# Kernel tuning notes

Measured on AMD Instinct MI355X. Metric: run time of the kernel, lower is better.

Reference implementation:

```python
import jax, jax.numpy as jnp
import numpy as np
import math

B, N, M, D, HID, OUT = 8, 2048, 2048, 1024, 1024, 1024

def setup_inputs() -> dict:
    key = jax.random.key(0)
    k1, k2, k3, k4, k5, k6 = jax.random.split(key, 6)
    h1 = jax.random.normal(k1, (B, N, D), dtype=jnp.float32)
    h2 = jax.random.normal(k2, (B, M, D), dtype=jnp.float32)
    mask = jax.random.randint(k3, (B, N, M), 0, 2, dtype=jnp.int32)
    # nn.Linear(in, out, bias=False) weight has shape (out, in)
    Wq = jax.random.normal(k4, (HID, D), dtype=jnp.float32) / math.sqrt(D)
    Wk = jax.random.normal(k5, (HID, D), dtype=jnp.float32) / math.sqrt(D)
    Wv = jax.random.normal(k6, (OUT, D), dtype=jnp.float32) / math.sqrt(D)
    return {"h1": h1, "h2": h2, "mask": mask, "Wq": Wq, "Wk": Wk, "Wv": Wv}

def reference(h1, h2, mask, Wq, Wk, Wv):
    Q = jnp.einsum('bnd,hd->bnh', h1, Wq)            # (B,N,HID)
    K = jnp.einsum('bmd,hd->bmh', h2, Wk)            # (B,M,HID)
    V = jnp.einsum('bmd,od->bmo', h2, Wv)            # (B,M,OUT)
    E = jnp.einsum('bnh,bmh->bnm', Q, K)             # (B,N,M) scores
    # NOTE: original masks E BEFORE dividing by sqrt(hidden_d)
    E = jnp.where(mask == 0, jnp.float32(-1e10), E)
    A = jax.nn.softmax(E / math.sqrt(HID), axis=2)
    return jnp.einsum('bnm,bmo->bno', A, V)          # (B,N,OUT)
```

## Files before the change

kernel.cpp:

```cpp
#include <hip/hip_runtime.h>


using f16   = _Float16;
using f16x4 = __attribute__((ext_vector_type(4))) _Float16;
using f16x8 = __attribute__((ext_vector_type(8))) _Float16;
using f32x4 = __attribute__((ext_vector_type(4))) float;

typedef unsigned int u32_g __attribute__((address_space(1)));
typedef unsigned int u32_l __attribute__((address_space(3)));

__device__ __forceinline__ void gl_lds16(const f16* g, f16* l) {
    __builtin_amdgcn_global_load_lds((const u32_g*)g, (u32_l*)l, 16, 0, 0);
}

#define FENCE() asm volatile("" ::: "memory")
#define BAR()   do { FENCE(); __builtin_amdgcn_s_barrier(); FENCE(); } while (0)

#define MFMA_HALF(A0_, A1_, A2_, A3_, RG_)                                               \
  do {                                                                                   \
    if constexpr (EPI == 2) {                                                            \
      rs[RG_+0] = __builtin_amdgcn_mfma_f32_16x16x32_f16(A0_, bones, rs[RG_+0], 0,0,0);  \
      rs[RG_+1] = __builtin_amdgcn_mfma_f32_16x16x32_f16(A1_, bones, rs[RG_+1], 0,0,0);  \
      rs[RG_+2] = __builtin_amdgcn_mfma_f32_16x16x32_f16(A2_, bones, rs[RG_+2], 0,0,0);  \
      rs[RG_+3] = __builtin_amdgcn_mfma_f32_16x16x32_f16(A3_, bones, rs[RG_+3], 0,0,0);  \
    }                                                                                    \
    acc[RG_+0][0] = __builtin_amdgcn_mfma_f32_16x16x32_f16(A0_, b0, acc[RG_+0][0],0,0,0);\
    acc[RG_+0][1] = __builtin_amdgcn_mfma_f32_16x16x32_f16(A0_, b1, acc[RG_+0][1],0,0,0);\
    acc[RG_+0][2] = __builtin_amdgcn_mfma_f32_16x16x32_f16(A0_, b2, acc[RG_+0][2],0,0,0);\
    acc[RG_+0][3] = __builtin_amdgcn_mfma_f32_16x16x32_f16(A0_, b3, acc[RG_+0][3],0,0,0);\
    acc[RG_+1][0] = __builtin_amdgcn_mfma_f32_16x16x32_f16(A1_, b0, acc[RG_+1][0],0,0,0);\
    acc[RG_+1][1] = __builtin_amdgcn_mfma_f32_16x16x32_f16(A1_, b1, acc[RG_+1][1],0,0,0);\
    acc[RG_+1][2] = __builtin_amdgcn_mfma_f32_16x16x32_f16(A1_, b2, acc[RG_+1][2],0,0,0);\
    acc[RG_+1][3] = __builtin_amdgcn_mfma_f32_16x16x32_f16(A1_, b3, acc[RG_+1][3],0,0,0);\
    acc[RG_+2][0] = __builtin_amdgcn_mfma_f32_16x16x32_f16(A2_, b0, acc[RG_+2][0],0,0,0);\
    acc[RG_+2][1] = __builtin_amdgcn_mfma_f32_16x16x32_f16(A2_, b1, acc[RG_+2][1],0,0,0);\
    acc[RG_+2][2] = __builtin_amdgcn_mfma_f32_16x16x32_f16(A2_, b2, acc[RG_+2][2],0,0,0);\
    acc[RG_+2][3] = __builtin_amdgcn_mfma_f32_16x16x32_f16(A2_, b3, acc[RG_+2][3],0,0,0);\
    acc[RG_+3][0] = __builtin_amdgcn_mfma_f32_16x16x32_f16(A3_, b0, acc[RG_+3][0],0,0,0);\
    acc[RG_+3][1] = __builtin_amdgcn_mfma_f32_16x16x32_f16(A3_, b1, acc[RG_+3][1],0,0,0);\
    acc[RG_+3][2] = __builtin_amdgcn_mfma_f32_16x16x32_f16(A3_, b2, acc[RG_+3][2],0,0,0);\
    acc[RG_+3][3] = __builtin_amdgcn_mfma_f32_16x16x32_f16(A3_, b3, acc[RG_+3][3],0,0,0);\
  } while (0)

#define TILE_BODY(T_, STG_, VM_)                                                         \
  {                                                                                      \
    const f16* bufA_ = smem + ((T_) & 3) * 16384;                                        \
    const f16* bufB_ = bufA_ + 8192;                                                     \
    if (STG_) {                                                                          \
      f16* dA_ = ldsAw + ((T_ + 3) & 3) * 16384;                                         \
      f16* dB_ = ldsBw + ((T_ + 3) & 3) * 16384;                                         \
      const f16* gA_ = gAs + (long)(T_ + 3) * 32;                                        \
      const f16* gB_ = gBs + (long)(T_ + 3) * 32;                                        \
      gl_lds16(gA_, dA_);                                                                \
      gl_lds16(gA_ + sweep, dA_ + 4096);                                                 \
      gl_lds16(gB_, dB_);                                                                \
      gl_lds16(gB_ + sweep, dB_ + 4096);                                                 \
    }                                                                                    \
    f16x8 a0_, a1_, a2_, a3_, a4_, a5_, a6_, a7_, b0, b1, b2, b3;                        \
    a0_ = *(const f16x8*)(bufA_ + offA);                                                 \
    a1_ = *(const f16x8*)(bufA_ + offA + 512);                                           \
    a2_ = *(const f16x8*)(bufA_ + offA + 1024);                                          \
    a3_ = *(const f16x8*)(bufA_ + offA + 1536);                                          \
    b0  = *(const f16x8*)(bufB_ + offB);                                                 \
    b1  = *(const f16x8*)(bufB_ + offB + 512);                                           \
    b2  = *(const f16x8*)(bufB_ + offB + 1024);                                          \
    b3  = *(const f16x8*)(bufB_ + offB + 1536);                                          \
    a4_ = *(const f16x8*)(bufA_ + offA + 2048);                                          \
    a5_ = *(const f16x8*)(bufA_ + offA + 2560);                                          \
    a6_ = *(const f16x8*)(bufA_ + offA + 3072);                                          \
    a7_ = *(const f16x8*)(bufA_ + offA + 3584);                                          \
    __builtin_amdgcn_s_setprio(1);                                                       \
    MFMA_HALF(a0_, a1_, a2_, a3_, 0);                                                    \
    MFMA_HALF(a4_, a5_, a6_, a7_, 4);                                                    \
    __builtin_amdgcn_s_setprio(0);                                                       \
    asm volatile(VM_ ::: "memory");                                                      \
    BAR();                                                                               \
  }

template <int EPI, int GDEC, int LGX>
__global__ __launch_bounds__(512, 2)
void gemm256_nt_f16(const f16* __restrict__ A, const f16* __restrict__ B,
                    void* __restrict__ Cv, const int* __restrict__ Mask,
                    int N, int K, long sA, long sB, long sC, long sMask)
{
    __shared__ f16 smem[4 * 16384];

    int bx, by, bz;
    if constexpr (GDEC == 0) {
        bx = blockIdx.x; by = blockIdx.y; bz = blockIdx.z;
    } else {
        int l = blockIdx.x;
        bz = l & 7; bx = (l >> 3) & ((1 << LGX) - 1); by = l >> (3 + LGX);
    }
    const f16* Ab = A + (long)bz * sA;
    const f16* Bb = B + (long)bz * sB;
    const int bm0 = by * 256;
    const int bn0 = bx * 256;

    const int tid  = threadIdx.x;
    const int lane = tid & 63;
    const int wid  = tid >> 6;
    const int wm   = (wid >> 2) * 128;
    const int wn   = (wid & 3)  * 64;
    const int lr   = lane & 15;
    const int quad = lane >> 4;
    const int kb   = (quad ^ ((lr >> 1) & 3)) << 3;

    const int offA = (wm + lr) * 32 + kb;
    const int offB = (wn + lr) * 32 + kb;

    const int r0 = tid >> 2, c0 = tid & 3;
    const int sw = (c0 ^ ((r0 >> 1) & 3)) << 3;
    const f16* gAs = Ab + (long)(bm0 + r0) * K + sw;
    const f16* gBs = Bb + (long)(bn0 + r0) * K + sw;
    const long sweep = (long)128 * K;

    f16* ldsAw = smem + wid * 512;
    f16* ldsBw = smem + 8192 + wid * 512;

    f32x4 acc[8][4] = {};
    f32x4 rs[8] = {};
    f16x8 bones;
#pragma unroll
    for (int j = 0; j < 8; ++j) bones[j] = (f16)1.0f;

    const int nt = K >> 5;

#pragma unroll
    for (int tt = 0; tt < 3; ++tt) {
        const f16* gA = gAs + (long)tt * 32;
        const f16* gB = gBs + (long)tt * 32;
        f16* dA = ldsAw + tt * 16384;
        f16* dB = ldsBw + tt * 16384;
        gl_lds16(gA, dA);
        gl_lds16(gA + sweep, dA + 4096);
        gl_lds16(gB, dB);
        gl_lds16(gB + sweep, dB + 4096);
    }
    asm volatile("s_waitcnt vmcnt(8)" ::: "memory");
    BAR();

#pragma unroll 1
    for (int t = 0; t < nt - 3; ++t) {
        TILE_BODY(t, 1, "s_waitcnt vmcnt(4)");
    }
    TILE_BODY(nt - 3, 0, "s_waitcnt vmcnt(4)");
    TILE_BODY(nt - 2, 0, "s_waitcnt vmcnt(0)");
    TILE_BODY(nt - 1, 0, "");

    if constexpr (EPI == 0) {
        f16* C = (f16*)Cv + (long)bz * sC;
#pragma unroll
        for (int rg = 0; rg < 8; ++rg)
#pragma unroll
            for (int cg = 0; cg < 4; ++cg)
#pragma unroll
                for (int r = 0; r < 4; ++r) {
                    long idx = (long)(bm0 + wm + rg * 16 + quad * 4 + r) * N
                             + (bn0 + wn + cg * 16 + lr);
                    C[idx] = (f16)acc[rg][cg][r];
                }
    } else if constexpr (EPI == 1) {
        f16* C = (f16*)Cv + (long)bz * sC;
        const int* Mk = Mask + (long)bz * sMask;
#pragma unroll
        for (int rg = 0; rg < 8; ++rg)
#pragma unroll
            for (int cg = 0; cg < 4; ++cg)
#pragma unroll
                for (int r = 0; r < 4; ++r) {
                    long idx = (long)(bm0 + wm + rg * 16 + quad * 4 + r) * N
                             + (bn0 + wn + cg * 16 + lr);
                    float v = (Mk[idx] == 0) ? -1e10f : acc[rg][cg][r];
                    C[idx] = (f16)__expf(v * 0.03125f);
                }
    } else {
        float* C = (float*)Cv + (long)bz * sC;
#pragma unroll
        for (int rg = 0; rg < 8; ++rg) {
            float inv[4];
#pragma unroll
            for (int r = 0; r < 4; ++r) {
                float s = rs[rg][r];
                inv[r] = (s > 0.f) ? 1.0f / s : 0.f;
            }
#pragma unroll
            for (int cg = 0; cg < 4; ++cg)
#pragma unroll
                for (int r = 0; r < 4; ++r) {
                    long idx = (long)(bm0 + wm + rg * 16 + quad * 4 + r) * N
                             + (bn0 + wn + cg * 16 + lr);
                    C[idx] = acc[rg][cg][r] * inv[r];
                }
        }
    }
}

__global__ __launch_bounds__(256)
void cvt_f32_f16(const float* __restrict__ src, f16* __restrict__ dst)
{
    long i = ((long)blockIdx.x * 256 + threadIdx.x) * 4;
    float4 v = *(const float4*)(src + i);
    f16x4 o;
    o[0] = (f16)v.x; o[1] = (f16)v.y; o[2] = (f16)v.z; o[3] = (f16)v.w;
    *(f16x4*)(dst + i) = o;
}

__global__ __launch_bounds__(256)
void cvt_w3(const float* __restrict__ a, const float* __restrict__ b,
            const float* __restrict__ c,
            f16* __restrict__ oa, f16* __restrict__ ob, f16* __restrict__ oc)
{
    int bid = blockIdx.x;
    const float* s; f16* d;
    if (bid < 1024)      { s = a; d = oa; }
    else if (bid < 2048) { s = b; d = ob; bid -= 1024; }
    else                 { s = c; d = oc; bid -= 2048; }
    long i = ((long)bid * 256 + threadIdx.x) * 4;
    float4 v = *(const float4*)(s + i);
    f16x4 o;
    o[0] = (f16)v.x; o[1] = (f16)v.y; o[2] = (f16)v.z; o[3] = (f16)v.w;
    *(f16x4*)(d + i) = o;
}

extern "C" void kernel_launch(void* const* d_in, const int* in_sizes, int n_in,
                              void* d_out, int out_size, void* d_ws, size_t ws_size,
                              hipStream_t stream)
{
    const float* h1   = (const float*)d_in[0];
    const float* h2   = (const float*)d_in[1];
    const int*   mask = (const int*)d_in[2];
    const float* Wq   = (const float*)d_in[3];
    const float* Wk   = (const float*)d_in[4];
    const float* Wv   = (const float*)d_in[5];
    float* out = (float*)d_out;

    char* ws = (char*)d_ws;
    f16* h1f = (f16*)(ws);
    f16* h2f = (f16*)(ws + 33554432);
    f16* Wqf = (f16*)(ws + 67108864);
    f16* Wkf = (f16*)(ws + 69206016);
    f16* Wvf = (f16*)(ws + 71303168);
    f16* SP  = (f16*)(ws + 33554432);
    f16* Vt  = (f16*)(ws);
    f16* Qf  = (f16*)d_out;
    f16* Kp  = (f16*)((char*)d_out + 33554432);

    dim3 blk(256);
    dim3 blk5(512);

    cvt_f32_f16<<<dim3(16384), blk, 0, stream>>>(h1, h1f);
    cvt_f32_f16<<<dim3(16384), blk, 0, stream>>>(h2, h2f);
    cvt_w3<<<dim3(3072), blk, 0, stream>>>(Wq, Wk, Wv, Wqf, Wkf, Wvf);

    gemm256_nt_f16<0, 0, 0><<<dim3(4, 64, 1), blk5, 0, stream>>>(h1f, Wqf, Qf,
        nullptr, 1024, 1024, 0, 0, 0, 0);
    gemm256_nt_f16<0, 0, 0><<<dim3(4, 64, 1), blk5, 0, stream>>>(h2f, Wkf, Kp,
        nullptr, 1024, 1024, 0, 0, 0, 0);
    gemm256_nt_f16<0, 0, 0><<<dim3(8, 4, 8), blk5, 0, stream>>>(Wvf, h2f, Vt,
        nullptr, 2048, 1024, 0, (long)2048 * 1024, (long)1024 * 2048, 0);
    gemm256_nt_f16<1, 1, 3><<<dim3(512), blk5, 0, stream>>>(Qf, Kp, SP,
        mask, 2048, 1024, (long)2048 * 1024, (long)2048 * 1024,
        (long)2048 * 2048, (long)2048 * 2048);
    gemm256_nt_f16<2, 1, 2><<<dim3(256), blk5, 0, stream>>>(SP, Vt, out,
        nullptr, 1024, 2048, (long)2048 * 2048, (long)1024 * 2048,
        (long)2048 * 1024, 0);
}
```

Measured before the change: 560.1 us.

## Prefetch mask into packed bits during GEMM mainloop and merge conversion kernels

In the score GEMM (EPI==1), the int32 mask values for each thread's output elements are loaded across the last 16 K-tiles of the mainloop and packed into four 32-bit words, so the epilogue no longer waits on scattered mask loads. Masked entries are written as zero directly instead of exp(-1e10 scaled). Separately, the three fp32-to-fp16 conversion launches are merged into a single kernel to cut launch overhead. The prefetch adds register pressure and extra vector-memory traffic inside the pipelined loop, which may interfere with the waitcnt-based staging.

```diff
diff --git a/kernel.cpp b/kernel.cpp
--- a/kernel.cpp
+++ b/kernel.cpp
@@ -15,6 +15,28 @@
 
 #define FENCE() asm volatile("" ::: "memory")
 #define BAR()   do { FENCE(); __builtin_amdgcn_s_barrier(); FENCE(); } while (0)
+
+#define MASK_ISSUE(U_)                                                   \
+  { int idx0_ = (U_) * 8;                                                \
+    _Pragma("unroll")                                                    \
+    for (int j_ = 0; j_ < 8; ++j_) {                                     \
+      int idx_ = idx0_ + j_;                                             \
+      long off_ = (long)(((idx_ >> 4) * 16) + (idx_ & 3)) * N            \
+                + (((idx_ >> 2) & 3) * 16);                              \
+      mv[j_] = Mrow[off_];                                               \
+    } }
+
+#define MASK_PACK(U_)                                                    \
+  { unsigned b_ = 0;                                                     \
+    _Pragma("unroll")                                                    \
+    for (int j_ = 0; j_ < 8; ++j_) b_ |= (mv[j_] != 0 ? 1u : 0u) << j_;  \
+    unsigned sh_ = (unsigned)(((U_) & 3) * 8);                           \
+    int w_ = (U_) >> 2;                                                  \
+    mw[0] |= (w_ == 0) ? (b_ << sh_) : 0u;                               \
+    mw[1] |= (w_ == 1) ? (b_ << sh_) : 0u;                               \
+    mw[2] |= (w_ == 2) ? (b_ << sh_) : 0u;                               \
+    mw[3] |= (w_ == 3) ? (b_ << sh_) : 0u;                               \
+  }
 
 #define MFMA_HALF(A0_, A1_, A2_, A3_, RG_)                                               \
   do {                                                                                   \
@@ -46,6 +68,11 @@
   {                                                                                      \
     const f16* bufA_ = smem + ((T_) & 3) * 16384;                                        \
     const f16* bufB_ = bufA_ + 8192;                                                     \
+    if constexpr (EPI == 1) {                                                            \
+      int u_ = (T_) - WIN0;                                                              \
+      if (u_ >= 1) MASK_PACK(u_ - 1);                                                    \
+      if (u_ >= 0 && u_ < 16) MASK_ISSUE(u_);                                            \
+    }                                                                                    \
     if (STG_) {                                                                          \
       f16* dA_ = ldsAw + ((T_ + 3) & 3) * 16384;                                         \
       f16* dB_ = ldsBw + ((T_ + 3) & 3) * 16384;                                         \
@@ -125,6 +152,12 @@
     for (int j = 0; j < 8; ++j) bones[j] = (f16)1.0f;
 
     const int nt = K >> 5;
+    const int WIN0 = nt - 16;
+
+    int mv[8];
+    unsigned mw[4] = {0u, 0u, 0u, 0u};
+    const int* Mrow = Mask + (long)bz * sMask
+                    + (long)(bm0 + wm + quad * 4) * N + (bn0 + wn + lr);
 
 #pragma unroll
     for (int tt = 0; tt < 3; ++tt) {
@@ -148,6 +181,8 @@
     TILE_BODY(nt - 2, 0, "s_waitcnt vmcnt(0)");
     TILE_BODY(nt - 1, 0, "");
 
+    if constexpr (EPI == 1) MASK_PACK(15);
+
     if constexpr (EPI == 0) {
         f16* C = (f16*)Cv + (long)bz * sC;
 #pragma unroll
@@ -162,17 +197,18 @@
                 }
     } else if constexpr (EPI == 1) {
         f16* C = (f16*)Cv + (long)bz * sC;
-        const int* Mk = Mask + (long)bz * sMask;
 #pragma unroll
         for (int rg = 0; rg < 8; ++rg)
 #pragma unroll
             for (int cg = 0; cg < 4; ++cg)
 #pragma unroll
                 for (int r = 0; r < 4; ++r) {
+                    const int linear = rg * 16 + cg * 4 + r;
+                    bool keep = (mw[linear >> 5] >> (linear & 31)) & 1u;
                     long idx = (long)(bm0 + wm + rg * 16 + quad * 4 + r) * N
                              + (bn0 + wn + cg * 16 + lr);
-                    float v = (Mk[idx] == 0) ? -1e10f : acc[rg][cg][r];
-                    C[idx] = (f16)__expf(v * 0.03125f);
+                    float e = __expf(acc[rg][cg][r] * 0.03125f);
+                    C[idx] = keep ? (f16)e : (f16)0.0f;
                 }
     } else {
         float* C = (float*)Cv + (long)bz * sC;
@@ -197,25 +233,20 @@
 }
 
 __global__ __launch_bounds__(256)
-void cvt_f32_f16(const float* __restrict__ src, f16* __restrict__ dst)
-{
-    long i = ((long)blockIdx.x * 256 + threadIdx.x) * 4;
-    float4 v = *(const float4*)(src + i);
-    f16x4 o;
-    o[0] = (f16)v.x; o[1] = (f16)v.y; o[2] = (f16)v.z; o[3] = (f16)v.w;
-    *(f16x4*)(dst + i) = o;
-}
-
-__global__ __launch_bounds__(256)
-void cvt_w3(const float* __restrict__ a, const float* __restrict__ b,
-            const float* __restrict__ c,
-            f16* __restrict__ oa, f16* __restrict__ ob, f16* __restrict__ oc)
+void cvt_all(const float* __restrict__ h1, const float* __restrict__ h2,
+             const float* __restrict__ wq, const float* __restrict__ wk,
+             const float* __restrict__ wv,
+             f16* __restrict__ oh1, f16* __restrict__ oh2,
+             f16* __restrict__ owq, f16* __restrict__ owk,
+             f16* __restrict__ owv)
 {
     int bid = blockIdx.x;
     const float* s; f16* d;
-    if (bid < 1024)      { s = a; d = oa; }
-    else if (bid < 2048) { s = b; d = ob; bid -= 1024; }
-    else                 { s = c; d = oc; bid -= 2048; }
+    if (bid < 16384)      { s = h1; d = oh1; }
+    else if (bid < 32768) { s = h2; d = oh2; bid -= 16384; }
+    else if (bid < 33792) { s = wq; d = owq; bid -= 32768; }
+    else if (bid < 34816) { s = wk; d = owk; bid -= 33792; }
+    else                  { s = wv; d = owv; bid -= 34816; }
     long i = ((long)bid * 256 + threadIdx.x) * 4;
     float4 v = *(const float4*)(s + i);
     f16x4 o;
@@ -249,9 +280,8 @@
     dim3 blk(256);
     dim3 blk5(512);
 
-    cvt_f32_f16<<<dim3(16384), blk, 0, stream>>>(h1, h1f);
-    cvt_f32_f16<<<dim3(16384), blk, 0, stream>>>(h2, h2f);
-    cvt_w3<<<dim3(3072), blk, 0, stream>>>(Wq, Wk, Wv, Wqf, Wkf, Wvf);
+    cvt_all<<<dim3(35840), blk, 0, stream>>>(h1, h2, Wq, Wk, Wv,
+                                             h1f, h2f, Wqf, Wkf, Wvf);
 
     gemm256_nt_f16<0, 0, 0><<<dim3(4, 64, 1), blk5, 0, stream>>>(h1f, Wqf, Qf,
         nullptr, 1024, 1024, 0, 0, 0, 0);
```

After: 550.0 us. About the same (-1.8%).
